# Performance work log

Measured on AMD Instinct MI355X. Metric: run time of the kernel, lower is better.

## Reference

```python
import jax, jax.numpy as jnp
import numpy as np

IN_FEATURES = 2048
OUT_FEATURES = 50257
IGNORE_INDEX = -100
Z_REG = 1e-4
LOGIT_SCALE = 1.0


def setup_inputs() -> dict:
    key = jax.random.key(0)
    kx, kw, kl = jax.random.split(key, 3)
    x = jax.random.normal(kx, (2, 2048, IN_FEATURES), dtype=jnp.float32)
    # nn.init.normal_(weight, std=1/sqrt(in_features)), shape [V, d]
    weight = jax.random.normal(kw, (OUT_FEATURES, IN_FEATURES), dtype=jnp.float32) / jnp.sqrt(
        jnp.float32(IN_FEATURES))
    labels = jax.random.randint(kl, (2, 2048), 0, OUT_FEATURES, dtype=jnp.int64)
    return {"x": x, "labels": labels, "weight": weight}


def reference(x, labels, weight):
    # logits = x @ W.T, cast to fp32, scaled  -> [B, S, V]
    logits = jnp.einsum("bsd,vd->bsv", x, weight).astype(jnp.float32) * LOGIT_SCALE
    V = logits.shape[-1]
    flat_logits = logits.reshape(-1, V)            # [N, V]
    flat_labels = labels.reshape(-1)               # [N]

    valid = flat_labels != IGNORE_INDEX            # [N] bool
    n_valid = jnp.sum(valid.astype(jnp.float32))

    lse = jax.scipy.special.logsumexp(flat_logits, axis=-1)          # [N]
    safe_labels = jnp.where(valid, flat_labels, 0)
    picked = jnp.take_along_axis(flat_logits, safe_labels[:, None], axis=-1)[:, 0]
    nll = lse - picked                                               # [N]

    denom = jnp.maximum(n_valid, 1.0)
    loss = jnp.sum(jnp.where(valid, nll, 0.0)) / denom
    if Z_REG > 0.0:
        z_reg = jnp.sum(jnp.where(valid, lse * lse, 0.0)) / denom
        loss = jnp.where(n_valid > 0, loss + Z_REG * z_reg, loss)
    return loss
```

## Files before the change

### kernel.cpp

```cpp
#include <hip/hip_runtime.h>
#include <hip/hip_fp8.h>
#include <cmath>
#include <cstdint>

#define M_TOTAL 4096
#define K_DIM   2048
#define V_DIM   50257
#define V_PAD   50432
#define NVB     197
#define NKB     (K_DIM / 32)
#define BK      128
#define NKT     (K_DIM / BK)
#define NWG     (NVB * 16)
#define IGNORE_IDX (-100)
#define Z_REG 1e-4f

typedef int    i32x4 __attribute__((ext_vector_type(4)));
typedef int    i32x8 __attribute__((ext_vector_type(8)));
typedef float  f32x4 __attribute__((ext_vector_type(4)));
typedef __bf16 bf16_t;
typedef bf16_t bf16x4 __attribute__((ext_vector_type(4)));
typedef bf16_t bf16x8 __attribute__((ext_vector_type(8)));

typedef const __attribute__((address_space(1))) void g_cvoid;
typedef __attribute__((address_space(3))) void l_void;

__device__ __forceinline__ void gll16(const void* g, void* l) {
    __builtin_amdgcn_global_load_lds((g_cvoid*)(uintptr_t)g,
                                     (l_void*)(uint32_t)(uintptr_t)l, 16, 0, 0);
}

__global__ __launch_bounds__(256)
void cvt_f32_fp8mx(const float* __restrict__ src, uint8_t* __restrict__ dq,
                   uint8_t* __restrict__ sT, int rows_valid, int rows_pad)
{
    const long long nthread = (long long)rows_pad * NKB * 8;
    const long long stride  = (long long)gridDim.x * 256;
    for (long long g = (long long)blockIdx.x * 256 + threadIdx.x; g < nthread;
         g += stride) {
        const long long blk = g >> 3;
        const int sub = (int)(g & 7);
        const int row = (int)(blk >> 6);
        const int kb  = (int)(blk & 63);
        f32x4 v = {0.f, 0.f, 0.f, 0.f};
        if (row < rows_valid)
            v = *(const f32x4*)(src + (size_t)row * K_DIM + kb * 32 + sub * 4);
        float m = fmaxf(fmaxf(fabsf(v.x), fabsf(v.y)),
                        fmaxf(fabsf(v.z), fabsf(v.w)));
        m = fmaxf(m, __shfl_xor(m, 1, 64));
        m = fmaxf(m, __shfl_xor(m, 2, 64));
        m = fmaxf(m, __shfl_xor(m, 4, 64));
        const int eb = (int)((__float_as_uint(m) >> 23) & 0xff);
        uint32_t wq = 0u;
        int sbyte = 0;
        if (eb != 0) {
            const int E = min(max(eb - 135, -127), 120);
            sbyte = E + 127;
            const float mult = __uint_as_float((uint32_t)(127 - E) << 23);
            const float q0 = fminf(fmaxf(v.x * mult, -448.f), 448.f);
            const float q1 = fminf(fmaxf(v.y * mult, -448.f), 448.f);
            const float q2 = fminf(fmaxf(v.z * mult, -448.f), 448.f);
            const float q3 = fminf(fmaxf(v.w * mult, -448.f), 448.f);
            const __hip_fp8_e4m3 f0(q0), f1(q1), f2(q2), f3(q3);
            wq = (uint32_t)f0.__x | ((uint32_t)f1.__x << 8)
               | ((uint32_t)f2.__x << 16) | ((uint32_t)f3.__x << 24);
        }
        ((uint32_t*)dq)[blk * 8 + sub] = wq;
        if (sub == 0) sT[(size_t)kb * rows_pad + row] = (uint8_t)sbyte;
    }
}

__global__ __launch_bounds__(512, 2)
void lce_gemm_fp8(const uint8_t* __restrict__ Xq, const uint8_t* __restrict__ Wq,
                  const uint8_t* __restrict__ sAT, const uint8_t* __restrict__ sBT,
                  float* __restrict__ pm, float* __restrict__ ps)
{
    __shared__ __align__(16) uint8_t As[2][256 * BK];
    __shared__ __align__(16) uint8_t Bs[2][256 * BK];

    const int bid = blockIdx.x;
    const int wg  = (bid & 7) * (NWG / 8) + (bid >> 3);
    const int vb  = wg >> 4;
    const int mb  = wg & 15;
    const int m0  = mb * 256;
    const int v0  = vb * 256;

    const int tid  = threadIdx.x;
    const int lane = tid & 63;
    const int wave = tid >> 6;
    const int wr   = wave >> 2;
    const int wc   = wave & 3;
    const int lo4  = lane & 15;
    const int hi2  = lane >> 4;
    const int sw   = lo4 & 7;

    const int l7 = lane & 7, l3 = lane >> 3;
    const int scol = ((l7 ^ l3) << 4);
    const int srow = wave * 8 + l3;
    const uint8_t* baseA = Xq + (size_t)(m0 + srow) * K_DIM + scol;
    const uint8_t* baseB = Wq + (size_t)(v0 + srow) * K_DIM + scol;
    char* ldsA_w = (char*)&As[0][0] + wave * 1024;
    char* ldsB_w = (char*)&Bs[0][0] + wave * 1024;

#define STAGE(tt) do { const int _b = ((tt) & 1) * 32768;                    \
        const size_t _k = (size_t)(tt) * BK;                                 \
        _Pragma("unroll")                                                    \
        for (int u = 0; u < 4; ++u) {                                        \
            gll16(baseA + (size_t)u * 64 * K_DIM + _k, ldsA_w + _b + u * 8192);\
            gll16(baseB + (size_t)u * 64 * K_DIM + _k, ldsB_w + _b + u * 8192);\
        } } while (0)

#define RD8(dst_, base_, rowbase_) do {                                      \
        const char* _p = (base_) + ((rowbase_) + lo4) * 128;                 \
        const i32x4 _lo = *(const i32x4*)(_p + (((hi2 << 1) | 0) ^ sw) * 16);\
        const i32x4 _hi = *(const i32x4*)(_p + (((hi2 << 1) | 1) ^ sw) * 16);\
        dst_[0] = _lo[0]; dst_[1] = _lo[1]; dst_[2] = _lo[2]; dst_[3] = _lo[3];\
        dst_[4] = _hi[0]; dst_[5] = _hi[1]; dst_[6] = _hi[2]; dst_[7] = _hi[3];\
    } while (0)

    f32x4 acc[8][4];
    #pragma unroll
    for (int m = 0; m < 8; ++m)
        #pragma unroll
        for (int n = 0; n < 4; ++n) {
            f32x4 z = {0.f, 0.f, 0.f, 0.f};
            acc[m][n] = z;
        }

    STAGE(0);
    asm volatile("s_waitcnt vmcnt(0)" ::: "memory");
    __builtin_amdgcn_s_barrier();

    for (int t = 0; t < NKT; ++t) {
        const char* Ab = (const char*)&As[0][0] + (t & 1) * 32768;
        const char* Bb = (const char*)&Bs[0][0] + (t & 1) * 32768;
        if (t + 1 < NKT) STAGE(t + 1);

        const uint8_t* sA = sAT + (size_t)(t * 4 + hi2) * M_TOTAL + m0 + wr * 128 + lo4;
        const uint8_t* sB = sBT + (size_t)(t * 4 + hi2) * V_PAD  + v0 + wc * 64  + lo4;

        i32x8 bf[4];  int sb[4];
        #pragma unroll
        for (int n = 0; n < 4; ++n) { RD8(bf[n], Bb, wc * 64 + n * 16); sb[n] = sB[n * 16]; }

        i32x8 af[4];  int sa[4];
        #pragma unroll
        for (int m = 0; m < 4; ++m) { RD8(af[m], Ab, wr * 128 + m * 16); sa[m] = sA[m * 16]; }
        __builtin_amdgcn_s_setprio(1);
        #pragma unroll
        for (int m = 0; m < 4; ++m)
            #pragma unroll
            for (int n = 0; n < 4; ++n)
                acc[m][n] = __builtin_amdgcn_mfma_scale_f32_16x16x128_f8f6f4(
                    af[m], bf[n], acc[m][n], 0, 0, 0, sa[m], 0, sb[n]);
        __builtin_amdgcn_s_setprio(0);

        #pragma unroll
        for (int m = 0; m < 4; ++m) { RD8(af[m], Ab, wr * 128 + 64 + m * 16); sa[m] = sA[64 + m * 16]; }
        __builtin_amdgcn_s_setprio(1);
        #pragma unroll
        for (int m = 0; m < 4; ++m)
            #pragma unroll
            for (int n = 0; n < 4; ++n)
                acc[4 + m][n] = __builtin_amdgcn_mfma_scale_f32_16x16x128_f8f6f4(
                    af[m], bf[n], acc[4 + m][n], 0, 0, 0, sa[m], 0, sb[n]);
        __builtin_amdgcn_s_setprio(0);

        if (t + 1 < NKT) asm volatile("s_waitcnt vmcnt(0)" ::: "memory");
        __builtin_amdgcn_s_barrier();
    }
#undef STAGE
#undef RD8

    float* scrM = (float*)&As[0][0];
    float* scrS = scrM + 1024;
    #pragma unroll
    for (int m = 0; m < 8; ++m) {
        #pragma unroll
        for (int j = 0; j < 4; ++j) {
            float v_[4];
            float vmax = -INFINITY;
            #pragma unroll
            for (int n = 0; n < 4; ++n) {
                const int gcol = v0 + wc * 64 + n * 16 + lo4;
                const float v  = acc[m][n][j];
                v_[n] = (gcol < V_DIM) ? v : -INFINITY;
                vmax = fmaxf(vmax, v_[n]);
            }
            #pragma unroll
            for (int d = 1; d < 16; d <<= 1)
                vmax = fmaxf(vmax, __shfl_xor(vmax, d, 64));
            float s = 0.f;
            if (vmax > -INFINITY) {
                #pragma unroll
                for (int n = 0; n < 4; ++n) s += __expf(v_[n] - vmax);
                #pragma unroll
                for (int d = 1; d < 16; d <<= 1)
                    s += __shfl_xor(s, d, 64);
            }
            if (lo4 == 0) {
                const int row = wr * 128 + m * 16 + hi2 * 4 + j;
                scrM[row * 4 + wc] = vmax;
                scrS[row * 4 + wc] = s;
            }
        }
    }
    __syncthreads();
    if (tid < 256) {
        float M = -INFINITY;
        #pragma unroll
        for (int w4 = 0; w4 < 4; ++w4) M = fmaxf(M, scrM[tid * 4 + w4]);
        float S = 0.f;
        #pragma unroll
        for (int w4 = 0; w4 < 4; ++w4) {
            const float mm = scrM[tid * 4 + w4];
            if (mm > -INFINITY) S += scrS[tid * 4 + w4] * __expf(mm - M);
        }
        const size_t idx = (size_t)vb * M_TOTAL + m0 + tid;
        pm[idx] = M;
        ps[idx] = S;
    }
}

__global__ __launch_bounds__(256)
void lce_picked_f32(const float* __restrict__ x, const float* __restrict__ w,
                    const int* __restrict__ labels, float* __restrict__ picked)
{
    const int wv  = threadIdx.x >> 6, ln = threadIdx.x & 63;
    const int row = blockIdx.x * 4 + wv;
    const int lbl = labels[row];
    float s = 0.f;
    if (lbl != IGNORE_IDX) {
        const float* xr = x + (size_t)row * K_DIM;
        const float* wr = w + (size_t)lbl * K_DIM;
        #pragma unroll
        for (int c = 0; c < 8; ++c) {
            const f32x4 a = *(const f32x4*)(xr + c * 256 + ln * 4);
            const f32x4 b = *(const f32x4*)(wr + c * 256 + ln * 4);
            s += a.x * b.x + a.y * b.y + a.z * b.z + a.w * b.w;
        }
    }
    #pragma unroll
    for (int d = 32; d; d >>= 1) s += __shfl_down(s, d, 64);
    if (ln == 0) picked[row] = s;
}

__global__ __launch_bounds__(256)
void lce_row_reduce(const float* __restrict__ pm, const float* __restrict__ ps,
                    const float* __restrict__ picked, const int* __restrict__ labels,
                    float* __restrict__ pb)
{
    const int r   = blockIdx.x * 256 + threadIdx.x;
    const int lbl = labels[r];
    float nll = 0.f, zsq = 0.f, val = 0.f;
    if (lbl != IGNORE_IDX) {
        float M = -INFINITY;
        for (int c = 0; c < NVB; ++c)
            M = fmaxf(M, pm[(size_t)c * M_TOTAL + r]);
        float S = 0.f;
        for (int c = 0; c < NVB; ++c) {
            const float mc = pm[(size_t)c * M_TOTAL + r];
            if (mc > -INFINITY) S += ps[(size_t)c * M_TOTAL + r] * expf(mc - M);
        }
        const float lse = M + logf(S);
        nll = lse - picked[r];
        zsq = lse * lse;
        val = 1.f;
    }
    #pragma unroll
    for (int d = 32; d; d >>= 1) {
        nll += __shfl_down(nll, d, 64);
        zsq += __shfl_down(zsq, d, 64);
        val += __shfl_down(val, d, 64);
    }
    __shared__ float red[3][4];
    const int wv = threadIdx.x >> 6, ln = threadIdx.x & 63;
    if (ln == 0) { red[0][wv] = nll; red[1][wv] = zsq; red[2][wv] = val; }
    __syncthreads();
    if (threadIdx.x == 0) {
        float a = 0.f, b = 0.f, c_ = 0.f;
        #pragma unroll
        for (int i = 0; i < 4; ++i) { a += red[0][i]; b += red[1][i]; c_ += red[2][i]; }
        pb[blockIdx.x * 3 + 0] = a;
        pb[blockIdx.x * 3 + 1] = b;
        pb[blockIdx.x * 3 + 2] = c_;
    }
}

__global__ void lce_finalize(const float* __restrict__ pb, float* __restrict__ out)
{
    float a = 0.f, b = 0.f, c_ = 0.f;
    for (int i = 0; i < 16; ++i) {
        a  += pb[i * 3 + 0];
        b  += pb[i * 3 + 1];
        c_ += pb[i * 3 + 2];
    }
    const float denom = fmaxf(c_, 1.f);
    float loss = a / denom;
    if (c_ > 0.f) loss += Z_REG * (b / denom);
    out[0] = loss;
}

#define FVC 1024
#define FNCHUNK 50
#define FBK 64
#define LDSPAD 72
__device__ inline bf16x4 cvt4(f32x4 v) {
    bf16x4 r;
    r.x = (bf16_t)v.x; r.y = (bf16_t)v.y; r.z = (bf16_t)v.z; r.w = (bf16_t)v.w;
    return r;
}
__global__ __launch_bounds__(256)
void lce_gemm_stats_fused(const float* __restrict__ X, const float* __restrict__ W,
                          const int* __restrict__ labels,
                          float* __restrict__ pm, float* __restrict__ ps,
                          float* __restrict__ pp)
{
    __shared__ bf16_t As[128][LDSPAD];
    __shared__ bf16_t Bsh[128][LDSPAD];
    __shared__ float  sm[128], ss[128], sp[128];
    __shared__ float  part_m[2][128], part_s[2][128];
    __shared__ int    slab[128];

    const int bx    = blockIdx.x;
    const int chunk = bx >> 5;
    const int mb    = bx & 31;
    const int m0    = mb * 128;
    const int v0    = chunk * FVC;
    const int tid   = threadIdx.x;
    const int lane  = tid & 63;
    const int wave  = tid >> 6;
    const int wr    = wave >> 1;
    const int wc    = wave & 1;
    const int lo4   = lane & 15;
    const int hi2   = lane >> 4;
    const int sr0   = tid >> 4;
    const int sc4   = tid & 15;

    if (tid < 128) {
        sm[tid] = -INFINITY; ss[tid] = 0.f; sp[tid] = 0.f;
        slab[tid] = labels[m0 + tid];
    }
    __syncthreads();

    const int ncols = min(FVC, V_DIM - v0);
    const int nt    = (ncols + 127) >> 7;

    for (int vt = 0; vt < nt; ++vt) {
        f32x4 acc[4][4];
        #pragma unroll
        for (int m = 0; m < 4; ++m)
            #pragma unroll
            for (int n = 0; n < 4; ++n) {
                f32x4 z = {0.f, 0.f, 0.f, 0.f};
                acc[m][n] = z;
            }
        const int vrow0 = v0 + vt * 128;
        for (int kt = 0; kt < K_DIM / FBK; ++kt) {
            #pragma unroll
            for (int i = 0; i < 8; ++i) {
                const int row = i * 16 + sr0;
                const f32x4 va = *(const f32x4*)(X + (size_t)(m0 + row) * K_DIM + kt * FBK + sc4 * 4);
                *(bf16x4*)&As[row][sc4 * 4] = cvt4(va);
                const int grow = vrow0 + row;
                f32x4 vb = {0.f, 0.f, 0.f, 0.f};
                if (grow < V_DIM)
                    vb = *(const f32x4*)(W + (size_t)grow * K_DIM + kt * FBK + sc4 * 4);
                *(bf16x4*)&Bsh[row][sc4 * 4] = cvt4(vb);
            }
            __syncthreads();
            #pragma unroll
            for (int ks = 0; ks < 2; ++ks) {
                bf16x8 af[4], bfr[4];
                #pragma unroll
                for (int m = 0; m < 4; ++m)
                    af[m] = *(const bf16x8*)&As[wr * 64 + m * 16 + lo4][ks * 32 + hi2 * 8];
                #pragma unroll
                for (int n = 0; n < 4; ++n)
                    bfr[n] = *(const bf16x8*)&Bsh[wc * 64 + n * 16 + lo4][ks * 32 + hi2 * 8];
                #pragma unroll
                for (int m = 0; m < 4; ++m)
                    #pragma unroll
                    for (int n = 0; n < 4; ++n)
                        acc[m][n] = __builtin_amdgcn_mfma_f32_16x16x32_bf16(af[m], bfr[n], acc[m][n], 0, 0, 0);
            }
            __syncthreads();
        }
        const int vbase = vrow0 + wc * 64;
        #pragma unroll
        for (int m = 0; m < 4; ++m) {
            #pragma unroll
            for (int j = 0; j < 4; ++j) {
                const int rloc = wr * 64 + m * 16 + hi2 * 4 + j;
                const int lb   = slab[rloc];
                float vmax = -INFINITY;
                float v_[4];
                #pragma unroll
                for (int n = 0; n < 4; ++n) {
                    const int gcol = vbase + n * 16 + lo4;
                    const float v  = acc[m][n][j];
                    const bool ok  = (gcol < V_DIM);
                    v_[n] = ok ? v : -INFINITY;
                    if (ok && gcol == lb) sp[rloc] = v;
                    vmax = fmaxf(vmax, v_[n]);
                }
                #pragma unroll
                for (int d = 1; d < 16; d <<= 1)
                    vmax = fmaxf(vmax, __shfl_xor(vmax, d, 64));
                float s = 0.f;
                #pragma unroll
                for (int n = 0; n < 4; ++n) s += __expf(v_[n] - vmax);
                #pragma unroll
                for (int d = 1; d < 16; d <<= 1) s += __shfl_xor(s, d, 64);
                if (lo4 == 0) { part_m[wc][rloc] = vmax; part_s[wc][rloc] = s; }
            }
        }
        __syncthreads();
        if (tid < 128) {
            const float om  = sm[tid], os = ss[tid];
            const float m0_ = part_m[0][tid], s0 = part_s[0][tid];
            const float m1_ = part_m[1][tid], s1 = part_s[1][tid];
            const float nm  = fmaxf(om, fmaxf(m0_, m1_));
            float ns = 0.f;
            if (om  > -INFINITY) ns += os * __expf(om  - nm);
            if (m0_ > -INFINITY) ns += s0 * __expf(m0_ - nm);
            if (m1_ > -INFINITY) ns += s1 * __expf(m1_ - nm);
            sm[tid] = nm; ss[tid] = ns;
        }
    }
    __syncthreads();
    if (tid < 128) {
        const size_t idx = (size_t)chunk * M_TOTAL + (m0 + tid);
        pm[idx] = sm[tid]; ps[idx] = ss[tid]; pp[idx] = sp[tid];
    }
}

__global__ __launch_bounds__(256)
void lce_row_reduce_f(const float* __restrict__ pm, const float* __restrict__ ps,
                      const float* __restrict__ pp, const int* __restrict__ labels,
                      float* __restrict__ pb)
{
    const int r   = blockIdx.x * 256 + threadIdx.x;
    const int lbl = labels[r];
    float nll = 0.f, zsq = 0.f, val = 0.f;
    if (lbl != IGNORE_IDX) {
        float M = -INFINITY;
        for (int c = 0; c < FNCHUNK; ++c)
            M = fmaxf(M, pm[(size_t)c * M_TOTAL + r]);
        float S = 0.f, P = 0.f;
        for (int c = 0; c < FNCHUNK; ++c) {
            const float mc = pm[(size_t)c * M_TOTAL + r];
            if (mc > -INFINITY) S += ps[(size_t)c * M_TOTAL + r] * expf(mc - M);
            P += pp[(size_t)c * M_TOTAL + r];
        }
        const float lse = M + logf(S);
        nll = lse - P; zsq = lse * lse; val = 1.f;
    }
    #pragma unroll
    for (int d = 32; d; d >>= 1) {
        nll += __shfl_down(nll, d, 64);
        zsq += __shfl_down(zsq, d, 64);
        val += __shfl_down(val, d, 64);
    }
    __shared__ float red[3][4];
    const int wv = threadIdx.x >> 6, ln = threadIdx.x & 63;
    if (ln == 0) { red[0][wv] = nll; red[1][wv] = zsq; red[2][wv] = val; }
    __syncthreads();
    if (threadIdx.x == 0) {
        float a = 0.f, b = 0.f, c_ = 0.f;
        #pragma unroll
        for (int i = 0; i < 4; ++i) { a += red[0][i]; b += red[1][i]; c_ += red[2][i]; }
        pb[blockIdx.x * 3 + 0] = a;
        pb[blockIdx.x * 3 + 1] = b;
        pb[blockIdx.x * 3 + 2] = c_;
    }
}

extern "C" void kernel_launch(void* const* d_in, const int* in_sizes, int n_in,
                              void* d_out, int out_size, void* d_ws, size_t ws_size,
                              hipStream_t stream)
{
    const float* x      = (const float*)d_in[0];
    const int*   labels = (const int*)d_in[1];
    const float* w      = (const float*)d_in[2];
    float*       out    = (float*)d_out;

    const size_t wq_b   = (size_t)V_PAD * K_DIM;
    const size_t xq_b   = (size_t)M_TOTAL * K_DIM;
    const size_t sbt_b  = (size_t)NKB * V_PAD;
    const size_t sat_b  = (size_t)NKB * M_TOTAL;
    const size_t stat_n = (size_t)NVB * M_TOTAL;

    size_t off = 0;
    auto take = [&](size_t bytes) { size_t o = off; off += (bytes + 255) & ~(size_t)255; return o; };
    const size_t o_wq  = take(wq_b);
    const size_t o_xq  = take(xq_b);
    const size_t o_sbt = take(sbt_b);
    const size_t o_sat = take(sat_b);
    const size_t o_pm  = take(stat_n * sizeof(float));
    const size_t o_ps  = take(stat_n * sizeof(float));
    const size_t o_pk  = take(M_TOTAL * sizeof(float));
    const size_t o_pb  = take(16 * 3 * sizeof(float));
    const size_t need  = off;

    if (ws_size >= need) {
        uint8_t* Wq  = (uint8_t*)d_ws + o_wq;
        uint8_t* Xq  = (uint8_t*)d_ws + o_xq;
        uint8_t* sBT = (uint8_t*)d_ws + o_sbt;
        uint8_t* sAT = (uint8_t*)d_ws + o_sat;
        float* pm     = (float*)((char*)d_ws + o_pm);
        float* ps     = (float*)((char*)d_ws + o_ps);
        float* picked = (float*)((char*)d_ws + o_pk);
        float* pb     = (float*)((char*)d_ws + o_pb);

        cvt_f32_fp8mx<<<dim3(4096), dim3(256), 0, stream>>>(w, Wq, sBT, V_DIM, V_PAD);
        cvt_f32_fp8mx<<<dim3(1024), dim3(256), 0, stream>>>(x, Xq, sAT, M_TOTAL, M_TOTAL);
        lce_gemm_fp8<<<dim3(NWG), dim3(512), 0, stream>>>(Xq, Wq, sAT, sBT, pm, ps);
        lce_picked_f32<<<dim3(1024), dim3(256), 0, stream>>>(x, w, labels, picked);
        lce_row_reduce<<<dim3(16), dim3(256), 0, stream>>>(pm, ps, picked, labels, pb);
        lce_finalize<<<dim3(1), dim3(1), 0, stream>>>(pb, out);
    } else {
        const size_t fstat_n = (size_t)FNCHUNK * M_TOTAL;
        float* pm = (float*)d_ws;
        float* ps = pm + fstat_n;
        float* pp = ps + fstat_n;
        float* pb = pp + fstat_n;
        lce_gemm_stats_fused<<<dim3(FNCHUNK * 32), dim3(256), 0, stream>>>(
            x, w, labels, pm, ps, pp);
        lce_row_reduce_f<<<dim3(16), dim3(256), 0, stream>>>(pm, ps, pp, labels, pb);
        lce_finalize<<<dim3(1), dim3(1), 0, stream>>>(pb, out);
    }
}
```

Baseline: 842.0 us.

## Switch to 32x32x64 scaled MFMA with BK=64 four-slot LDS pipeline

Replaces the 16x16x128 scaled FP8 MFMA tiles with 32x32x64 tiles. It halves the K-tile to 64 and uses a four-slot LDS ring with a prefetch distance of two, waiting on partial vmcnt instead of draining all loads each iteration. LDS rows now pack two matrix rows per 128-byte line under a new XOR swizzle, and the logsumexp epilogue is remapped to the 32x32 accumulator layout. The FP8 quantizer also bumps the shared exponent when the scaled block maximum would exceed 448, which avoids clipping. The aim is better MFMA efficiency and more global-load latency hiding, at the cost of more barriers per K and a more intricate layout.

Result: slower. 1.085 ms (+28.8%).

```diff
diff --git a/kernel.cpp b/kernel.cpp
--- a/kernel.cpp
+++ b/kernel.cpp
@@ -9,15 +9,16 @@
 #define V_PAD   50432
 #define NVB     197
 #define NKB     (K_DIM / 32)
-#define BK      128
+#define BK      64
 #define NKT     (K_DIM / BK)
 #define NWG     (NVB * 16)
 #define IGNORE_IDX (-100)
 #define Z_REG 1e-4f
 
-typedef int    i32x4 __attribute__((ext_vector_type(4)));
-typedef int    i32x8 __attribute__((ext_vector_type(8)));
-typedef float  f32x4 __attribute__((ext_vector_type(4)));
+typedef int    i32x4  __attribute__((ext_vector_type(4)));
+typedef int    i32x8  __attribute__((ext_vector_type(8)));
+typedef float  f32x4  __attribute__((ext_vector_type(4)));
+typedef float  f32x16 __attribute__((ext_vector_type(16)));
 typedef __bf16 bf16_t;
 typedef bf16_t bf16x4 __attribute__((ext_vector_type(4)));
 typedef bf16_t bf16x8 __attribute__((ext_vector_type(8)));
@@ -54,9 +55,10 @@
         uint32_t wq = 0u;
         int sbyte = 0;
         if (eb != 0) {
-            const int E = min(max(eb - 135, -127), 120);
+            int E = min(max(eb - 135, -126), 119);
+            float mult = __uint_as_float((uint32_t)(127 - E) << 23);
+            if (m * mult > 448.f) { E += 1; mult *= 0.5f; }
             sbyte = E + 127;
-            const float mult = __uint_as_float((uint32_t)(127 - E) << 23);
             const float q0 = fminf(fmaxf(v.x * mult, -448.f), 448.f);
             const float q1 = fminf(fmaxf(v.y * mult, -448.f), 448.f);
             const float q2 = fminf(fmaxf(v.z * mult, -448.f), 448.f);
@@ -75,8 +77,8 @@
                   const uint8_t* __restrict__ sAT, const uint8_t* __restrict__ sBT,
                   float* __restrict__ pm, float* __restrict__ ps)
 {
-    __shared__ __align__(16) uint8_t As[2][256 * BK];
-    __shared__ __align__(16) uint8_t Bs[2][256 * BK];
+    __shared__ __align__(16) uint8_t As[4][256 * BK];
+    __shared__ __align__(16) uint8_t Bs[4][256 * BK];
 
     const int bid = blockIdx.x;
     const int wg  = (bid & 7) * (NWG / 8) + (bid >> 3);
@@ -90,116 +92,120 @@
     const int wave = tid >> 6;
     const int wr   = wave >> 2;
     const int wc   = wave & 3;
-    const int lo4  = lane & 15;
-    const int hi2  = lane >> 4;
-    const int sw   = lo4 & 7;
+    const int l31  = lane & 31;
+    const int ln5  = lane >> 5;
+
+    const int rh  = l31 >> 1;
+    const int x7  = rh & 7;
+    const int sb_ = ((lane & 1) << 2) | (ln5 << 1);
+    const int sA0 = ((sb_    ) ^ x7) << 4;
+    const int sA1 = ((sb_ | 1) ^ x7) << 4;
 
     const int l7 = lane & 7, l3 = lane >> 3;
-    const int scol = ((l7 ^ l3) << 4);
-    const int srow = wave * 8 + l3;
+    const int s0 = l7 ^ l3;
+    const int srow = (wave << 4) + (l3 << 1) + (s0 >> 2);
+    const int scol = (s0 & 3) << 4;
     const uint8_t* baseA = Xq + (size_t)(m0 + srow) * K_DIM + scol;
     const uint8_t* baseB = Wq + (size_t)(v0 + srow) * K_DIM + scol;
     char* ldsA_w = (char*)&As[0][0] + wave * 1024;
     char* ldsB_w = (char*)&Bs[0][0] + wave * 1024;
-
-#define STAGE(tt) do { const int _b = ((tt) & 1) * 32768;                    \
-        const size_t _k = (size_t)(tt) * BK;                                 \
-        _Pragma("unroll")                                                    \
-        for (int u = 0; u < 4; ++u) {                                        \
-            gll16(baseA + (size_t)u * 64 * K_DIM + _k, ldsA_w + _b + u * 8192);\
-            gll16(baseB + (size_t)u * 64 * K_DIM + _k, ldsB_w + _b + u * 8192);\
-        } } while (0)
-
-#define RD8(dst_, base_, rowbase_) do {                                      \
-        const char* _p = (base_) + ((rowbase_) + lo4) * 128;                 \
-        const i32x4 _lo = *(const i32x4*)(_p + (((hi2 << 1) | 0) ^ sw) * 16);\
-        const i32x4 _hi = *(const i32x4*)(_p + (((hi2 << 1) | 1) ^ sw) * 16);\
-        dst_[0] = _lo[0]; dst_[1] = _lo[1]; dst_[2] = _lo[2]; dst_[3] = _lo[3];\
-        dst_[4] = _hi[0]; dst_[5] = _hi[1]; dst_[6] = _hi[2]; dst_[7] = _hi[3];\
+    const size_t U1 = (size_t)128 * K_DIM;
+
+#define STAGE(tt) do { const int _s = (tt) & 3;                             \
+        const size_t _k = (size_t)(tt) * BK;                                \
+        gll16(baseA + _k,      ldsA_w + _s * 16384);                        \
+        gll16(baseA + _k + U1, ldsA_w + _s * 16384 + 8192);                 \
+        gll16(baseB + _k,      ldsB_w + _s * 16384);                        \
+        gll16(baseB + _k + U1, ldsB_w + _s * 16384 + 8192);                 \
     } while (0)
 
-    f32x4 acc[8][4];
+#define RDOP(dst_, slot_, rowbase_) do {                                    \
+        const char* _p = (slot_) + (((rowbase_) + rh) << 7);                \
+        const i32x4 _lo = *(const i32x4*)(_p + sA0);                        \
+        const i32x4 _hi = *(const i32x4*)(_p + sA1);                        \
+        dst_[0]=_lo[0]; dst_[1]=_lo[1]; dst_[2]=_lo[2]; dst_[3]=_lo[3];     \
+        dst_[4]=_hi[0]; dst_[5]=_hi[1]; dst_[6]=_hi[2]; dst_[7]=_hi[3];     \
+    } while (0)
+
+#define VM4  asm volatile("s_waitcnt vmcnt(4)" ::: "memory")
+#define VM0  asm volatile("s_waitcnt vmcnt(0)" ::: "memory")
+#define BAR  __builtin_amdgcn_s_barrier()
+
+    f32x16 acc[4][2];
     #pragma unroll
-    for (int m = 0; m < 8; ++m)
-        #pragma unroll
-        for (int n = 0; n < 4; ++n) {
-            f32x4 z = {0.f, 0.f, 0.f, 0.f};
-            acc[m][n] = z;
-        }
-
-    STAGE(0);
-    asm volatile("s_waitcnt vmcnt(0)" ::: "memory");
-    __builtin_amdgcn_s_barrier();
+    for (int m = 0; m < 4; ++m)
+        #pragma unroll
+        for (int n = 0; n < 2; ++n)
+            #pragma unroll
+            for (int j = 0; j < 16; ++j) acc[m][n][j] = 0.f;
+
+    STAGE(0); STAGE(1);
+    VM4;
+    BAR;
 
     for (int t = 0; t < NKT; ++t) {
-        const char* Ab = (const char*)&As[0][0] + (t & 1) * 32768;
-        const char* Bb = (const char*)&Bs[0][0] + (t & 1) * 32768;
-        if (t + 1 < NKT) STAGE(t + 1);
-
-        const uint8_t* sA = sAT + (size_t)(t * 4 + hi2) * M_TOTAL + m0 + wr * 128 + lo4;
-        const uint8_t* sB = sBT + (size_t)(t * 4 + hi2) * V_PAD  + v0 + wc * 64  + lo4;
-
-        i32x8 bf[4];  int sb[4];
-        #pragma unroll
-        for (int n = 0; n < 4; ++n) { RD8(bf[n], Bb, wc * 64 + n * 16); sb[n] = sB[n * 16]; }
-
-        i32x8 af[4];  int sa[4];
-        #pragma unroll
-        for (int m = 0; m < 4; ++m) { RD8(af[m], Ab, wr * 128 + m * 16); sa[m] = sA[m * 16]; }
+        const char* Ab = (const char*)&As[0][0] + (t & 3) * 16384;
+        const char* Bb = (const char*)&Bs[0][0] + (t & 3) * 16384;
+
+        const uint8_t* sA = sAT + (size_t)(t * 2 + ln5) * M_TOTAL + m0 + wr * 128 + l31;
+        const uint8_t* sB = sBT + (size_t)(t * 2 + ln5) * V_PAD  + v0 + wc * 64  + l31;
+        int sa[4], sbv[2];
+        #pragma unroll
+        for (int m = 0; m < 4; ++m) sa[m]  = sA[m * 32];
+        #pragma unroll
+        for (int n = 0; n < 2; ++n) sbv[n] = sB[n * 32];
+
+        if (t + 2 < NKT) STAGE(t + 2);
+
+        i32x8 af[4], bf[2];
+        #pragma unroll
+        for (int n = 0; n < 2; ++n) RDOP(bf[n], Bb, wc * 32 + n * 16);
+        #pragma unroll
+        for (int m = 0; m < 4; ++m) RDOP(af[m], Ab, wr * 64 + m * 16);
+
         __builtin_amdgcn_s_setprio(1);
         #pragma unroll
         for (int m = 0; m < 4; ++m)
             #pragma unroll
-            for (int n = 0; n < 4; ++n)
-                acc[m][n] = __builtin_amdgcn_mfma_scale_f32_16x16x128_f8f6f4(
-                    af[m], bf[n], acc[m][n], 0, 0, 0, sa[m], 0, sb[n]);
+            for (int n = 0; n < 2; ++n)
+                acc[m][n] = __builtin_amdgcn_mfma_scale_f32_32x32x64_f8f6f4(
+                    af[m], bf[n], acc[m][n], 0, 0, 0, sa[m], 0, sbv[n]);
         __builtin_amdgcn_s_setprio(0);
 
-        #pragma unroll
-        for (int m = 0; m < 4; ++m) { RD8(af[m], Ab, wr * 128 + 64 + m * 16); sa[m] = sA[64 + m * 16]; }
-        __builtin_amdgcn_s_setprio(1);
-        #pragma unroll
-        for (int m = 0; m < 4; ++m)
-            #pragma unroll
-            for (int n = 0; n < 4; ++n)
-                acc[4 + m][n] = __builtin_amdgcn_mfma_scale_f32_16x16x128_f8f6f4(
-                    af[m], bf[n], acc[4 + m][n], 0, 0, 0, sa[m], 0, sb[n]);
-        __builtin_amdgcn_s_setprio(0);
-
-        if (t + 1 < NKT) asm volatile("s_waitcnt vmcnt(0)" ::: "memory");
-        __builtin_amdgcn_s_barrier();
+        if (t + 3 < NKT)       VM4;
+        else if (t + 2 == NKT) VM0;
+        if (t + 1 < NKT)       BAR;
     }
 #undef STAGE
-#undef RD8
+#undef RDOP
+#undef VM4
+#undef VM0
+#undef BAR
 
     float* scrM = (float*)&As[0][0];
     float* scrS = scrM + 1024;
     #pragma unroll
-    for (int m = 0; m < 8; ++m) {
-        #pragma unroll
-        for (int j = 0; j < 4; ++j) {
-            float v_[4];
-            float vmax = -INFINITY;
-            #pragma unroll
-            for (int n = 0; n < 4; ++n) {
-                const int gcol = v0 + wc * 64 + n * 16 + lo4;
-                const float v  = acc[m][n][j];
-                v_[n] = (gcol < V_DIM) ? v : -INFINITY;
-                vmax = fmaxf(vmax, v_[n]);
-            }
-            #pragma unroll
-            for (int d = 1; d < 16; d <<= 1)
+    for (int m = 0; m < 4; ++m) {
+        #pragma unroll
+        for (int j = 0; j < 16; ++j) {
+            const int gc0 = v0 + wc * 64 + l31;
+            const int gc1 = gc0 + 32;
+            float va = (gc0 < V_DIM) ? acc[m][0][j] : -INFINITY;
+            float vb_ = (gc1 < V_DIM) ? acc[m][1][j] : -INFINITY;
+            float vmax = fmaxf(va, vb_);
+            #pragma unroll
+            for (int d = 1; d < 32; d <<= 1)
                 vmax = fmaxf(vmax, __shfl_xor(vmax, d, 64));
             float s = 0.f;
             if (vmax > -INFINITY) {
-                #pragma unroll
-                for (int n = 0; n < 4; ++n) s += __expf(v_[n] - vmax);
-                #pragma unroll
-                for (int d = 1; d < 16; d <<= 1)
+                s = ((gc0 < V_DIM) ? __expf(va - vmax) : 0.f)
+                  + ((gc1 < V_DIM) ? __expf(vb_ - vmax) : 0.f);
+                #pragma unroll
+                for (int d = 1; d < 32; d <<= 1)
                     s += __shfl_xor(s, d, 64);
             }
-            if (lo4 == 0) {
-                const int row = wr * 128 + m * 16 + hi2 * 4 + j;
+            if (l31 == 0) {
+                const int row = wr * 128 + m * 32 + (j & 3) + 8 * (j >> 2) + 4 * ln5;
                 scrM[row * 4 + wc] = vmax;
                 scrS[row * 4 + wc] = s;
             }
```

## Load A fragments directly from global and stage B scales in LDS

Applied to the files above, without the earlier changes.

The GEMM kernel stops staging the X (A) tile through shared memory. Each wave now reads its A fragments straight from global memory into registers, while only W (B) goes through LDS. The per-tile B scale bytes are also prefetched into a small LDS buffer instead of being read from global per lane. The quantizer gets a rounding fix that bumps the exponent when a scaled value would overflow 448. This halves LDS footprint and traffic, but A loads now hit global/L2 directly inside the MFMA loop with no prefetch, which risks exposing latency.

Result: slower. 1.330 ms (+58.0%).

```diff
diff --git a/kernel.cpp b/kernel.cpp
--- a/kernel.cpp
+++ b/kernel.cpp
@@ -54,9 +54,10 @@
         uint32_t wq = 0u;
         int sbyte = 0;
         if (eb != 0) {
-            const int E = min(max(eb - 135, -127), 120);
+            int E = min(max(eb - 135, -126), 119);
+            float mult = __uint_as_float((uint32_t)(127 - E) << 23);
+            if (m * mult > 448.f) { E += 1; mult *= 0.5f; }
             sbyte = E + 127;
-            const float mult = __uint_as_float((uint32_t)(127 - E) << 23);
             const float q0 = fminf(fmaxf(v.x * mult, -448.f), 448.f);
             const float q1 = fminf(fmaxf(v.y * mult, -448.f), 448.f);
             const float q2 = fminf(fmaxf(v.z * mult, -448.f), 448.f);
@@ -75,8 +76,8 @@
                   const uint8_t* __restrict__ sAT, const uint8_t* __restrict__ sBT,
                   float* __restrict__ pm, float* __restrict__ ps)
 {
-    __shared__ __align__(16) uint8_t As[2][256 * BK];
     __shared__ __align__(16) uint8_t Bs[2][256 * BK];
+    __shared__ __align__(16) uint8_t Ss[2][1024];
 
     const int bid = blockIdx.x;
     const int wg  = (bid & 7) * (NWG / 8) + (bid >> 3);
@@ -96,24 +97,27 @@
 
     const int l7 = lane & 7, l3 = lane >> 3;
     const int scol = ((l7 ^ l3) << 4);
-    const int srow = wave * 8 + l3;
-    const uint8_t* baseA = Xq + (size_t)(m0 + srow) * K_DIM + scol;
-    const uint8_t* baseB = Wq + (size_t)(v0 + srow) * K_DIM + scol;
-    char* ldsA_w = (char*)&As[0][0] + wave * 1024;
+    const uint8_t* baseB = Wq + (size_t)(v0 + wave * 8 + l3) * K_DIM + scol;
     char* ldsB_w = (char*)&Bs[0][0] + wave * 1024;
 
-#define STAGE(tt) do { const int _b = ((tt) & 1) * 32768;                    \
-        const size_t _k = (size_t)(tt) * BK;                                 \
-        _Pragma("unroll")                                                    \
-        for (int u = 0; u < 4; ++u) {                                        \
-            gll16(baseA + (size_t)u * 64 * K_DIM + _k, ldsA_w + _b + u * 8192);\
+    const uint8_t* baseSB = sBT + (size_t)(lane >> 4) * V_PAD + v0 + (lane & 15) * 16;
+
+    const uint8_t* aBase  = Xq + (size_t)(m0 + wr * 128 + lo4) * K_DIM + hi2 * 32;
+    const uint8_t* saBase = sAT + (size_t)hi2 * M_TOTAL + m0 + wr * 128 + lo4;
+
+#define STAGE_B(tt) do { const int _b = ((tt) & 1) * 32768;                   \
+        const size_t _k = (size_t)(tt) * BK;                                  \
+        _Pragma("unroll")                                                     \
+        for (int u = 0; u < 4; ++u)                                           \
             gll16(baseB + (size_t)u * 64 * K_DIM + _k, ldsB_w + _b + u * 8192);\
-        } } while (0)
-
-#define RD8(dst_, base_, rowbase_) do {                                      \
-        const char* _p = (base_) + ((rowbase_) + lo4) * 128;                 \
-        const i32x4 _lo = *(const i32x4*)(_p + (((hi2 << 1) | 0) ^ sw) * 16);\
-        const i32x4 _hi = *(const i32x4*)(_p + (((hi2 << 1) | 1) ^ sw) * 16);\
+        if (wave == 0)                                                        \
+            gll16(baseSB + (size_t)(tt) * 4 * V_PAD, &Ss[(tt) & 1][0]);       \
+    } while (0)
+
+#define RD8(dst_, base_, rowbase_) do {                                       \
+        const char* _p = (base_) + ((rowbase_) + lo4) * 128;                  \
+        const i32x4 _lo = *(const i32x4*)(_p + (((hi2 << 1) | 0) ^ sw) * 16); \
+        const i32x4 _hi = *(const i32x4*)(_p + (((hi2 << 1) | 1) ^ sw) * 16); \
         dst_[0] = _lo[0]; dst_[1] = _lo[1]; dst_[2] = _lo[2]; dst_[3] = _lo[3];\
         dst_[4] = _hi[0]; dst_[5] = _hi[1]; dst_[6] = _hi[2]; dst_[7] = _hi[3];\
     } while (0)
@@ -127,52 +131,49 @@
             acc[m][n] = z;
         }
 
-    STAGE(0);
+    STAGE_B(0);
     asm volatile("s_waitcnt vmcnt(0)" ::: "memory");
     __builtin_amdgcn_s_barrier();
 
     for (int t = 0; t < NKT; ++t) {
-        const char* Ab = (const char*)&As[0][0] + (t & 1) * 32768;
-        const char* Bb = (const char*)&Bs[0][0] + (t & 1) * 32768;
-        if (t + 1 < NKT) STAGE(t + 1);
-
-        const uint8_t* sA = sAT + (size_t)(t * 4 + hi2) * M_TOTAL + m0 + wr * 128 + lo4;
-        const uint8_t* sB = sBT + (size_t)(t * 4 + hi2) * V_PAD  + v0 + wc * 64  + lo4;
+        const char*    Bb   = (const char*)&Bs[0][0] + (t & 1) * 32768;
+        const uint8_t* sLds = &Ss[t & 1][0];
+        if (t + 1 < NKT) STAGE_B(t + 1);
 
         i32x8 bf[4];  int sb[4];
         #pragma unroll
-        for (int n = 0; n < 4; ++n) { RD8(bf[n], Bb, wc * 64 + n * 16); sb[n] = sB[n * 16]; }
-
-        i32x8 af[4];  int sa[4];
-        #pragma unroll
-        for (int m = 0; m < 4; ++m) { RD8(af[m], Ab, wr * 128 + m * 16); sa[m] = sA[m * 16]; }
+        for (int n = 0; n < 4; ++n) {
+            RD8(bf[n], Bb, wc * 64 + n * 16);
+            sb[n] = sLds[hi2 * 256 + wc * 64 + n * 16 + lo4];
+        }
+
+        const uint8_t* aT  = aBase  + t * 128;
+        const uint8_t* saT = saBase + (size_t)t * 4 * M_TOTAL;
+
         __builtin_amdgcn_s_setprio(1);
         #pragma unroll
-        for (int m = 0; m < 4; ++m)
+        for (int m = 0; m < 8; ++m) {
+            const char* ap = (const char*)(aT + (size_t)m * 16 * K_DIM);
+            const i32x4 alo = *(const i32x4*)(ap);
+            const i32x4 ahi = *(const i32x4*)(ap + 16);
+            i32x8 af;
+            af[0] = alo[0]; af[1] = alo[1]; af[2] = alo[2]; af[3] = alo[3];
+            af[4] = ahi[0]; af[5] = ahi[1]; af[6] = ahi[2]; af[7] = ahi[3];
+            const int sa = saT[(size_t)m * 16];
             #pragma unroll
             for (int n = 0; n < 4; ++n)
                 acc[m][n] = __builtin_amdgcn_mfma_scale_f32_16x16x128_f8f6f4(
-                    af[m], bf[n], acc[m][n], 0, 0, 0, sa[m], 0, sb[n]);
+                    af, bf[n], acc[m][n], 0, 0, 0, sa, 0, sb[n]);
+        }
         __builtin_amdgcn_s_setprio(0);
 
-        #pragma unroll
-        for (int m = 0; m < 4; ++m) { RD8(af[m], Ab, wr * 128 + 64 + m * 16); sa[m] = sA[64 + m * 16]; }
-        __builtin_amdgcn_s_setprio(1);
-        #pragma unroll
-        for (int m = 0; m < 4; ++m)
-            #pragma unroll
-            for (int n = 0; n < 4; ++n)
-                acc[4 + m][n] = __builtin_amdgcn_mfma_scale_f32_16x16x128_f8f6f4(
-                    af[m], bf[n], acc[4 + m][n], 0, 0, 0, sa[m], 0, sb[n]);
-        __builtin_amdgcn_s_setprio(0);
-
-        if (t + 1 < NKT) asm volatile("s_waitcnt vmcnt(0)" ::: "memory");
+        asm volatile("s_waitcnt vmcnt(0)" ::: "memory");
         __builtin_amdgcn_s_barrier();
     }
-#undef STAGE
+#undef STAGE_B
 #undef RD8
 
-    float* scrM = (float*)&As[0][0];
+    float* scrM = (float*)&Bs[0][0];
     float* scrS = scrM + 1024;
     #pragma unroll
     for (int m = 0; m < 8; ++m) {
```
